# Kernel tuning notes

Measured on AMD Instinct MI355X. Metric: run time of the kernel, lower is better.

## Reference

```python
import jax, jax.numpy as jnp
import numpy as np

B, T, V, C, H, HS, L, DFF = 8192, 8, 65, 512, 8, 64, 6, 2048
LN_EPS = 1e-5


def _layernorm(x, g, b):
    mu = jnp.mean(x, axis=-1, keepdims=True)
    var = jnp.mean(jnp.square(x - mu), axis=-1, keepdims=True)
    return (x - mu) * jax.lax.rsqrt(var + LN_EPS) * g + b


def setup_inputs() -> dict:
    key = jax.random.key(0)
    ks = jax.random.split(key, 16)
    s = 0.02
    inp = {
        "idx": jax.random.randint(ks[0], (B, T), 0, V),
        "tok_table": jax.random.normal(ks[1], (V, C), jnp.float32) * s,
        "pos_table": jax.random.normal(ks[2], (T, C), jnp.float32) * s,
        "wq": jax.random.normal(ks[3], (L, H, C, HS), jnp.float32) * s,
        "wk": jax.random.normal(ks[4], (L, H, C, HS), jnp.float32) * s,
        "wv": jax.random.normal(ks[5], (L, H, C, HS), jnp.float32) * s,
        "proj_w": jax.random.normal(ks[6], (L, C, C), jnp.float32) * s,
        "proj_b": jnp.zeros((L, C), jnp.float32),
        "w1": jax.random.normal(ks[7], (L, C, DFF), jnp.float32) * s,
        "b1": jnp.zeros((L, DFF), jnp.float32),
        "w2": jax.random.normal(ks[8], (L, DFF, C), jnp.float32) * s,
        "b2": jnp.zeros((L, C), jnp.float32),
        "ln1_g": jnp.ones((L, C), jnp.float32),
        "ln1_b": jnp.zeros((L, C), jnp.float32),
        "ln2_g": jnp.ones((L, C), jnp.float32),
        "ln2_b": jnp.zeros((L, C), jnp.float32),
        "lm_w": jax.random.normal(ks[9], (C, V), jnp.float32) * s,
        "lm_b": jnp.zeros((V,), jnp.float32),
    }
    return inp


def reference(idx, tok_table, pos_table, wq, wk, wv, proj_w, proj_b,
              w1, b1, w2, b2, ln1_g, ln1_b, ln2_g, ln2_b, lm_w, lm_b):
    idx = idx[:, -T:]
    x = tok_table[idx] + pos_table[None, :T, :]  # [B,T,C]
    mask = jnp.tril(jnp.ones((T, T), bool))
    scale = C ** (-0.5)  # NOTE: original scales by n_embed, not head_size
    for l in range(L):
        q = jnp.einsum('btc,hcd->bhtd', x, wq[l])
        k = jnp.einsum('btc,hcd->bhtd', x, wk[l])
        v = jnp.einsum('btc,hcd->bhtd', x, wv[l])
        att = jnp.einsum('bhtd,bhsd->bhts', q, k) * scale
        att = jnp.where(mask, att, -jnp.inf)
        att = jax.nn.softmax(att, axis=-1)
        o = jnp.einsum('bhts,bhsd->bhtd', att, v)
        o = o.transpose(0, 2, 1, 3).reshape(x.shape[0], T, C)  # concat heads
        o = o @ proj_w[l] + proj_b[l]
        x = _layernorm(x + o, ln1_g[l], ln1_b[l])  # post-norm
        h = jax.nn.relu(x @ w1[l] + b1[l]) @ w2[l] + b2[l]
        x = _layernorm(x + h, ln2_g[l], ln2_b[l])
    logits = x @ lm_w + lm_b  # [B,T,V]
    return logits
```

## Files before the change

kernel.cpp:

```cpp
#include <hip/hip_runtime.h>
#include <hip/hip_bf16.h>
#include <math.h>

#define NTOK  65536
#define CDIM  512
#define NHEAD 8
#define HSZ   64
#define NLAYER 6
#define DFF   2048
#define VOCAB 65

typedef unsigned short u16;
typedef __attribute__((ext_vector_type(8))) __bf16 bf16x8;
typedef __attribute__((ext_vector_type(4))) float f32x4;
typedef __attribute__((ext_vector_type(8))) unsigned short ushort8;

__device__ __forceinline__ float b2f(u16 u) {
    union { unsigned int i; float f; } x; x.i = ((unsigned int)u) << 16; return x.f;
}
__device__ __forceinline__ u16 f2b(float f) {
    union { float f; unsigned int i; } x; x.f = f;
    unsigned int r = x.i + 0x7fffu + ((x.i >> 16) & 1u);
    return (u16)(r >> 16);
}

__device__ __forceinline__ void async16(const u16* g, u16* l) {
    __builtin_amdgcn_global_load_lds(
        (const __attribute__((address_space(1))) void*)g,
        (__attribute__((address_space(3))) void*)l, 16, 0, 0);
}

template<int EPI>
__global__ __launch_bounds__(512)
void gemm_bt(const u16* __restrict__ A, const u16* __restrict__ Bt,
             void* __restrict__ Cout, const float* __restrict__ bias,
             const u16* __restrict__ res, int K, int lda, int N, int Nout)
{
    __shared__ u16 lA[2 * 256 * 32];
    __shared__ u16 lB[2 * 128 * 32];
    const int tid  = threadIdx.x;

    const int Nx = gridDim.x;
    const int id = blockIdx.y * Nx + blockIdx.x;
    const int xcd = id & 7;
    const int j0  = id >> 3;
    const int mt  = xcd + 8 * (j0 / Nx);
    const int nt  = j0 - (j0 / Nx) * Nx;
    const int m0  = mt * 256;
    const int n0  = nt * 128;

    const int lane = tid & 63;
    const int wv   = tid >> 6;
    const int wr   = (wv >> 1) * 64;
    const int wc   = (wv & 1) * 64;
    const int r16  = lane & 15;
    const int quad = lane >> 4;

    f32x4 acc[4][4] = {};

    const int srow = tid >> 2, skseg = (tid & 3) * 8;
    const u16* pA  = A  + (size_t)(m0 + srow) * lda + skseg;
    const u16* pA2 = pA + (size_t)128 * lda;
    const u16* pB  = Bt + (size_t)(n0 + srow) * K + skseg;
    u16* lAt = &lA[(size_t)tid * 8];
    u16* lBt = &lB[(size_t)tid * 8];

    for (int k0 = 0; k0 < K; k0 += 64) {
        async16(pA  + k0,      lAt);
        async16(pA2 + k0,      lAt + 4096);
        async16(pA  + k0 + 32, lAt + 8192);
        async16(pA2 + k0 + 32, lAt + 12288);
        async16(pB  + k0,      lBt);
        async16(pB  + k0 + 32, lBt + 4096);
        __syncthreads();

#pragma unroll
        for (int s = 0; s < 2; s++) {
            const u16* bA = &lA[s * 8192];
            const u16* bB = &lB[s * 4096];
            bf16x8 af[4], bfr[4];
#pragma unroll
            for (int i = 0; i < 4; i++)
                af[i] = *(const bf16x8*)(const void*)&bA[(wr + i * 16 + r16) * 32 + quad * 8];
#pragma unroll
            for (int j = 0; j < 4; j++)
                bfr[j] = *(const bf16x8*)(const void*)&bB[(wc + j * 16 + r16) * 32 + quad * 8];
#pragma unroll
            for (int j = 0; j < 4; j++)
#pragma unroll
                for (int i = 0; i < 4; i++)
                    acc[j][i] = __builtin_amdgcn_mfma_f32_16x16x32_bf16(bfr[j], af[i], acc[j][i], 0, 0, 0);
        }
        __syncthreads();
    }

#pragma unroll
    for (int i = 0; i < 4; i++) {
        const int row = m0 + wr + i * 16 + r16;
#pragma unroll
        for (int j = 0; j < 4; j++) {
            const int colb = n0 + wc + j * 16 + quad * 4;
            float v[4];
#pragma unroll
            for (int r = 0; r < 4; r++) v[r] = acc[j][i][r];
            if (EPI == 1 || EPI == 2) {
                const f32x4 b4 = *(const f32x4*)(const void*)&bias[colb];
#pragma unroll
                for (int r = 0; r < 4; r++) v[r] += b4[r];
            }
            if (EPI == 1) {
                const uint2 rv = *(const uint2*)(const void*)&res[(size_t)row * N + colb];
                v[0] += b2f((u16)(rv.x & 0xffffu));
                v[1] += b2f((u16)(rv.x >> 16));
                v[2] += b2f((u16)(rv.y & 0xffffu));
                v[3] += b2f((u16)(rv.y >> 16));
            }
            if (EPI == 2) {
#pragma unroll
                for (int r = 0; r < 4; r++) v[r] = fmaxf(v[r], 0.f);
            }
            if (EPI == 3) {
#pragma unroll
                for (int r = 0; r < 4; r++) {
                    const int col = colb + r;
                    if (col < Nout)
                        ((float*)Cout)[(size_t)row * Nout + col] = v[r] + bias[col];
                }
            } else {
                uint2 o;
                o.x = (unsigned)f2b(v[0]) | ((unsigned)f2b(v[1]) << 16);
                o.y = (unsigned)f2b(v[2]) | ((unsigned)f2b(v[3]) << 16);
                *(uint2*)(void*)&((u16*)Cout)[(size_t)row * N + colb] = o;
            }
        }
    }
}

__global__ __launch_bounds__(256)
void attn_k(u16* __restrict__ qkv)
{
    __shared__ float sq[4][8][65], sk[4][8][65], sv[4][8][65], sp[4][64];
    const int w = threadIdx.x >> 6, lane = threadIdx.x & 63;
    const int unit = blockIdx.x * 4 + w;
    const int b = unit >> 3, h = unit & 7;
    const size_t base = (size_t)b * 8 * 1536 + h * 64;
    {
        const int t = lane >> 3, d0 = (lane & 7) * 8;
        const ushort8 q8 = *(const ushort8*)(const void*)&qkv[base + t * 1536 + d0];
        const ushort8 k8 = *(const ushort8*)(const void*)&qkv[base + t * 1536 + 512 + d0];
        const ushort8 v8 = *(const ushort8*)(const void*)&qkv[base + t * 1536 + 1024 + d0];
#pragma unroll
        for (int i = 0; i < 8; i++) {
            sq[w][t][d0 + i] = b2f(q8[i]);
            sk[w][t][d0 + i] = b2f(k8[i]);
            sv[w][t][d0 + i] = b2f(v8[i]);
        }
    }
    __syncthreads();
    const int t = lane >> 3, s = lane & 7;
    float sc = -1e30f;
    if (s <= t) {
        float d = 0.f;
#pragma unroll
        for (int c = 0; c < 64; c++) d += sq[w][t][c] * sk[w][s][c];
        sc = d * 0.04419417382415922f;
    }
    float mx = sc;
#pragma unroll
    for (int m = 1; m < 8; m <<= 1) mx = fmaxf(mx, __shfl_xor(mx, m, 8));
    float e = __expf(sc - mx);
    if (s > t) e = 0.f;
    float sum = e;
#pragma unroll
    for (int m = 1; m < 8; m <<= 1) sum += __shfl_xor(sum, m, 8);
    sp[w][lane] = e / sum;
    __syncthreads();
    {
        const int tt = lane >> 3, d0 = (lane & 7) * 8;
        float a[8] = {};
#pragma unroll
        for (int ss = 0; ss < 8; ss++) {
            const float p = sp[w][tt * 8 + ss];
#pragma unroll
            for (int i = 0; i < 8; i++) a[i] += p * sv[w][ss][d0 + i];
        }
        ushort8 o;
#pragma unroll
        for (int i = 0; i < 8; i++) o[i] = f2b(a[i]);
        *(ushort8*)(void*)&qkv[base + tt * 1536 + d0] = o;
    }
}

__global__ __launch_bounds__(256)
void ln_k(const u16* __restrict__ y, const float* __restrict__ g,
          const float* __restrict__ be, u16* __restrict__ x)
{
    const int w = threadIdx.x >> 6, lane = threadIdx.x & 63;
    const size_t tok = (size_t)blockIdx.x * 4 + w;
    const u16* row = y + tok * 512 + lane * 8;
    ushort8 raw = *(const ushort8*)(const void*)row;
    float v[8];
#pragma unroll
    for (int i = 0; i < 8; i++) v[i] = b2f(raw[i]);
    float s = 0.f;
#pragma unroll
    for (int i = 0; i < 8; i++) s += v[i];
#pragma unroll
    for (int m = 1; m < 64; m <<= 1) s += __shfl_xor(s, m, 64);
    const float mu = s * (1.f / 512.f);
    float q = 0.f;
#pragma unroll
    for (int i = 0; i < 8; i++) { float d = v[i] - mu; q += d * d; }
#pragma unroll
    for (int m = 1; m < 64; m <<= 1) q += __shfl_xor(q, m, 64);
    const float inv = rsqrtf(q * (1.f / 512.f) + 1e-5f);
    f32x4 g0  = *(const f32x4*)(const void*)&g[lane * 8];
    f32x4 g1  = *(const f32x4*)(const void*)&g[lane * 8 + 4];
    f32x4 b0  = *(const f32x4*)(const void*)&be[lane * 8];
    f32x4 b1v = *(const f32x4*)(const void*)&be[lane * 8 + 4];
    ushort8 o;
#pragma unroll
    for (int i = 0; i < 4; i++) o[i]     = f2b((v[i] - mu) * inv * g0[i] + b0[i]);
#pragma unroll
    for (int i = 0; i < 4; i++) o[i + 4] = f2b((v[i + 4] - mu) * inv * g1[i] + b1v[i]);
    *(ushort8*)(void*)&x[tok * 512 + lane * 8] = o;
}

__global__ __launch_bounds__(256)
void embed_k(const int* __restrict__ idx, const float* __restrict__ tokt,
             const float* __restrict__ pos, u16* __restrict__ xb)
{
    const int gid = blockIdx.x * 256 + threadIdx.x;
    const int tk = gid >> 6, seg = (gid & 63) * 8;
    const int t = tk & 7;
    const int ix = idx[tk];
    const f32x4 a0 = *(const f32x4*)(const void*)&tokt[(size_t)ix * 512 + seg];
    const f32x4 a1 = *(const f32x4*)(const void*)&tokt[(size_t)ix * 512 + seg + 4];
    const f32x4 p0 = *(const f32x4*)(const void*)&pos[t * 512 + seg];
    const f32x4 p1 = *(const f32x4*)(const void*)&pos[t * 512 + seg + 4];
    ushort8 o;
#pragma unroll
    for (int i = 0; i < 4; i++) o[i]     = f2b(a0[i] + p0[i]);
#pragma unroll
    for (int i = 0; i < 4; i++) o[i + 4] = f2b(a1[i] + p1[i]);
    *(ushort8*)(void*)&xb[(size_t)tk * 512 + seg] = o;
}

__global__ __launch_bounds__(256)
void conv_t2_k(const float* __restrict__ in, u16* __restrict__ out, int K, int N)
{
    __shared__ float t[32][33];
    const int tx = threadIdx.x & 31, ty4 = (threadIdx.x >> 5) * 4;
    const int n0 = blockIdx.x * 32, k0 = blockIdx.y * 32, l = blockIdx.z;
    const size_t per = (size_t)K * N;
    const float* src = in + l * per;
#pragma unroll
    for (int r = 0; r < 4; r++)
        t[ty4 + r][tx] = src[(size_t)(k0 + ty4 + r) * N + n0 + tx];
    __syncthreads();
    u16* dst = out + l * per;
#pragma unroll
    for (int r = 0; r < 4; r++)
        dst[(size_t)(n0 + ty4 + r) * K + k0 + tx] = f2b(t[tx][ty4 + r]);
}

__global__ __launch_bounds__(256)
void conv_qkv2_k(const float* __restrict__ wq, const float* __restrict__ wk,
                 const float* __restrict__ wv, u16* __restrict__ out)
{
    __shared__ float t[32][33];
    const int tx = threadIdx.x & 31, ty4 = (threadIdx.x >> 5) * 4;
    const int c0 = blockIdx.x * 32, d0 = blockIdx.y * 32;
    const int z = blockIdx.z;
    const int sel = z / 48, rem = z - sel * 48;
    const int l = rem >> 3, h = rem & 7;
    const float* src = (sel == 0) ? wq : (sel == 1) ? wk : wv;
    const float* sb = src + (((size_t)l * 8 + h) * 512) * 64;
#pragma unroll
    for (int r = 0; r < 4; r++)
        t[ty4 + r][tx] = sb[(size_t)(c0 + ty4 + r) * 64 + d0 + tx];
    __syncthreads();
    u16* dst = out + (size_t)l * 786432 + (size_t)(sel * 512 + h * 64 + d0) * 512;
#pragma unroll
    for (int r = 0; r < 4; r++)
        dst[(size_t)(ty4 + r) * 512 + c0 + tx] = f2b(t[tx][ty4 + r]);
}

__global__ __launch_bounds__(256)
void conv_lm_k(const float* __restrict__ lm_w, u16* __restrict__ out)
{
    int gid = blockIdx.x * 256 + threadIdx.x;
    int n = gid >> 9, c = gid & 511;
    out[gid] = (n < VOCAB) ? f2b(lm_w[(size_t)c * VOCAB + n]) : (u16)0;
}

extern "C" void kernel_launch(void* const* d_in, const int* in_sizes, int n_in,
                              void* d_out, int out_size, void* d_ws, size_t ws_size,
                              hipStream_t stream)
{
    const int*   idx    = (const int*)  d_in[0];
    const float* tokt   = (const float*)d_in[1];
    const float* post   = (const float*)d_in[2];
    const float* wq     = (const float*)d_in[3];
    const float* wk     = (const float*)d_in[4];
    const float* wvp    = (const float*)d_in[5];
    const float* proj_w = (const float*)d_in[6];
    const float* proj_b = (const float*)d_in[7];
    const float* w1     = (const float*)d_in[8];
    const float* b1     = (const float*)d_in[9];
    const float* w2     = (const float*)d_in[10];
    const float* b2     = (const float*)d_in[11];
    const float* ln1_g  = (const float*)d_in[12];
    const float* ln1_b  = (const float*)d_in[13];
    const float* ln2_g  = (const float*)d_in[14];
    const float* ln2_b  = (const float*)d_in[15];
    const float* lm_w   = (const float*)d_in[16];
    const float* lm_b   = (const float*)d_in[17];
    float* out = (float*)d_out;

    char* ws = (char*)d_ws;
    u16* wqkvt = (u16*)(ws + 0);
    u16* wprjt = (u16*)(ws + 9437184);
    u16* ww1t  = (u16*)(ws + 12582912);
    u16* ww2t  = (u16*)(ws + 25165824);
    u16* wlmt  = (u16*)(ws + 37748736);
    u16* xb    = (u16*)(ws + 37879808);
    char* big  = ws + 104988672;

    const size_t fixed_bytes = 104988672ull;
    const size_t avail = (ws_size > fixed_bytes) ? (ws_size - fixed_bytes) : 0;
    int chunk_a = 8192, chunk_m = 8192;
    const int cands[3] = {65536, 32768, 16384};
    for (int i = 0; i < 3; i++)
        if ((size_t)cands[i] * 3072ull <= avail) { chunk_a = cands[i]; break; }
    for (int i = 0; i < 3; i++)
        if ((size_t)cands[i] * 4096ull <= avail) { chunk_m = cands[i]; break; }
    const int nca = NTOK / chunk_a, ncm = NTOK / chunk_m;
    u16* qkvc = (u16*)big;
    u16* h1c  = (u16*)big;

    conv_qkv2_k<<<dim3(16, 2, 144), 256, 0, stream>>>(wq, wk, wvp, wqkvt);
    conv_t2_k  <<<dim3(16, 16, 6), 256, 0, stream>>>(proj_w, wprjt, 512, 512);
    conv_t2_k  <<<dim3(64, 16, 6), 256, 0, stream>>>(w1, ww1t, 512, 2048);
    conv_t2_k  <<<dim3(16, 64, 6), 256, 0, stream>>>(w2, ww2t, 2048, 512);
    conv_lm_k  <<<128 * 512 / 256, 256, 0, stream>>>(lm_w, wlmt);

    embed_k<<<NTOK * 64 / 256, 256, 0, stream>>>(idx, tokt, post, xb);

    for (int l = 0; l < NLAYER; l++) {
        for (int c = 0; c < nca; c++) {
            const size_t t0 = (size_t)c * chunk_a;
            gemm_bt<0><<<dim3(12, chunk_a / 256), 512, 0, stream>>>(
                xb + t0 * 512, wqkvt + (size_t)l * 786432, qkvc,
                nullptr, nullptr, 512, 512, 1536, 1536);
            attn_k<<<chunk_a / 4, 256, 0, stream>>>(qkvc);
            gemm_bt<1><<<dim3(4, chunk_a / 256), 512, 0, stream>>>(
                qkvc, wprjt + (size_t)l * 262144, xb + t0 * 512,
                proj_b + l * 512, xb + t0 * 512, 512, 1536, 512, 512);
        }
        ln_k<<<NTOK / 4, 256, 0, stream>>>(xb, ln1_g + l * 512, ln1_b + l * 512, xb);
        for (int c = 0; c < ncm; c++) {
            const size_t t0 = (size_t)c * chunk_m;
            gemm_bt<2><<<dim3(16, chunk_m / 256), 512, 0, stream>>>(
                xb + t0 * 512, ww1t + (size_t)l * 1048576, h1c,
                b1 + l * 2048, nullptr, 512, 512, 2048, 2048);
            gemm_bt<1><<<dim3(4, chunk_m / 256), 512, 0, stream>>>(
                h1c, ww2t + (size_t)l * 1048576, xb + t0 * 512,
                b2 + l * 512, xb + t0 * 512, 2048, 2048, 512, 512);
        }
        ln_k<<<NTOK / 4, 256, 0, stream>>>(xb, ln2_g + l * 512, ln2_b + l * 512, xb);
    }

    gemm_bt<3><<<dim3(1, 256), 512, 0, stream>>>(
        xb, wlmt, out, lm_b, nullptr, 512, 512, 128, VOCAB);
}
```

Before: 3.910 ms.

## Add 256x256-tile GEMM with swizzled LDS, double-buffered prefetch and interleaved MFMA

```diff
diff --git a/kernel.cpp b/kernel.cpp
--- a/kernel.cpp
+++ b/kernel.cpp
@@ -30,76 +30,146 @@
         (__attribute__((address_space(3))) void*)l, 16, 0, 0);
 }
 
+template<int JB, int IB>
+__device__ __forceinline__ void mfma_quad(f32x4 (&acc)[4][8],
+                                          const bf16x8 (&af)[4][2],
+                                          const bf16x8 (&bf)[4][2])
+{
+#pragma unroll
+    for (int kk = 0; kk < 2; kk++)
+#pragma unroll
+        for (int j = 0; j < 2; j++)
+#pragma unroll
+            for (int i = 0; i < 4; i++)
+                acc[JB + j][IB + i] = __builtin_amdgcn_mfma_f32_16x16x32_bf16(
+                    bf[JB + j][kk], af[i][kk], acc[JB + j][IB + i], 0, 0, 0);
+}
+
 template<int EPI>
-__global__ __launch_bounds__(512)
-void gemm_bt(const u16* __restrict__ A, const u16* __restrict__ Bt,
-             void* __restrict__ Cout, const float* __restrict__ bias,
-             const u16* __restrict__ res, int K, int lda, int N, int Nout)
-{
-    __shared__ u16 lA[2 * 256 * 32];
-    __shared__ u16 lB[2 * 128 * 32];
-    const int tid  = threadIdx.x;
+__global__ __launch_bounds__(512, 2)
+void gemm256(const u16* __restrict__ A, const u16* __restrict__ Bt,
+             void* Cout, const float* __restrict__ bias,
+             const u16* res, int K, int lda, int N, int Nout)
+{
+    extern __shared__ __attribute__((aligned(16))) u16 lds[];
+    const int tid = threadIdx.x;
 
     const int Nx = gridDim.x;
     const int id = blockIdx.y * Nx + blockIdx.x;
     const int xcd = id & 7;
-    const int j0  = id >> 3;
-    const int mt  = xcd + 8 * (j0 / Nx);
-    const int nt  = j0 - (j0 / Nx) * Nx;
-    const int m0  = mt * 256;
-    const int n0  = nt * 128;
-
-    const int lane = tid & 63;
-    const int wv   = tid >> 6;
-    const int wr   = (wv >> 1) * 64;
-    const int wc   = (wv & 1) * 64;
-    const int r16  = lane & 15;
-    const int quad = lane >> 4;
-
-    f32x4 acc[4][4] = {};
-
-    const int srow = tid >> 2, skseg = (tid & 3) * 8;
-    const u16* pA  = A  + (size_t)(m0 + srow) * lda + skseg;
-    const u16* pA2 = pA + (size_t)128 * lda;
-    const u16* pB  = Bt + (size_t)(n0 + srow) * K + skseg;
-    u16* lAt = &lA[(size_t)tid * 8];
-    u16* lBt = &lB[(size_t)tid * 8];
-
-    for (int k0 = 0; k0 < K; k0 += 64) {
-        async16(pA  + k0,      lAt);
-        async16(pA2 + k0,      lAt + 4096);
-        async16(pA  + k0 + 32, lAt + 8192);
-        async16(pA2 + k0 + 32, lAt + 12288);
-        async16(pB  + k0,      lBt);
-        async16(pB  + k0 + 32, lBt + 4096);
-        __syncthreads();
-
-#pragma unroll
-        for (int s = 0; s < 2; s++) {
-            const u16* bA = &lA[s * 8192];
-            const u16* bB = &lB[s * 4096];
-            bf16x8 af[4], bfr[4];
-#pragma unroll
-            for (int i = 0; i < 4; i++)
-                af[i] = *(const bf16x8*)(const void*)&bA[(wr + i * 16 + r16) * 32 + quad * 8];
-#pragma unroll
-            for (int j = 0; j < 4; j++)
-                bfr[j] = *(const bf16x8*)(const void*)&bB[(wc + j * 16 + r16) * 32 + quad * 8];
-#pragma unroll
-            for (int j = 0; j < 4; j++)
-#pragma unroll
-                for (int i = 0; i < 4; i++)
-                    acc[j][i] = __builtin_amdgcn_mfma_f32_16x16x32_bf16(bfr[j], af[i], acc[j][i], 0, 0, 0);
-        }
-        __syncthreads();
-    }
-
-#pragma unroll
-    for (int i = 0; i < 4; i++) {
-        const int row = m0 + wr + i * 16 + r16;
+    const int j0 = id >> 3;
+    const int mt = xcd + 8 * (j0 / Nx);
+    const int nt = j0 - (j0 / Nx) * Nx;
+    const int m0 = mt * 256, n0 = nt * 256;
+
+    const int lane = tid & 63, wvv = tid >> 6;
+    const int wvm = wvv >> 2, wvn = wvv & 3;
+    const int r16 = lane & 15, quad = lane >> 4;
+    const int gk0 = quad ^ (r16 & 7);
+    const int g0x8 = gk0 * 8, g1x8 = (gk0 ^ 4) * 8;
+    const int arow = wvm * 128 + r16;
+    const int brow = wvn * 64 + r16;
+
+    const int srow = tid >> 3;
+    const int sg = (tid & 7) ^ (srow & 7);
+    const u16* pA = A + (size_t)(m0 + srow) * lda + sg * 8;
+    const u16* pB = Bt + (size_t)(n0 + srow) * K + sg * 8;
+    u16* const ldst = lds + tid * 8;
+    const size_t ldaq = (size_t)64 * lda, ldah = (size_t)128 * lda;
+    const size_t kq = (size_t)64 * K, kh = (size_t)128 * K;
+
+    const int nk = K >> 6;
+
+    f32x4 acc[4][8] = {};
+    bf16x8 af[4][2], bf[4][2];
+
+#define STAGE_A(c, kt, h) do { \
+    async16(pA + ((h) ? ldah : 0) + (size_t)((kt) * 64),        ldst + (c) * 32768 + (h) * 8192); \
+    async16(pA + ((h) ? ldah : 0) + ldaq + (size_t)((kt) * 64), ldst + (c) * 32768 + (h) * 8192 + 4096); } while (0)
+#define STAGE_B(c, kt, h) do { \
+    async16(pB + ((h) ? kh : 0) + (size_t)((kt) * 64),          ldst + (c) * 32768 + 16384 + (h) * 8192); \
+    async16(pB + ((h) ? kh : 0) + kq + (size_t)((kt) * 64),     ldst + (c) * 32768 + 16384 + (h) * 8192 + 4096); } while (0)
+#define LD_A4(IB0) do { _Pragma("unroll") \
+    for (int i = 0; i < 4; i++) { \
+        const int ro = cb + (arow + ((IB0) + i) * 16) * 64; \
+        af[i][0] = *(const bf16x8*)(const void*)&lds[ro + g0x8]; \
+        af[i][1] = *(const bf16x8*)(const void*)&lds[ro + g1x8]; \
+    } } while (0)
+#define LD_B2(JB0) do { _Pragma("unroll") \
+    for (int j = 0; j < 2; j++) { \
+        const int ro = cb + 16384 + (brow + ((JB0) + j) * 16) * 64; \
+        bf[(JB0) + j][0] = *(const bf16x8*)(const void*)&lds[ro + g0x8]; \
+        bf[(JB0) + j][1] = *(const bf16x8*)(const void*)&lds[ro + g1x8]; \
+    } } while (0)
+#define LGKM0() do { asm volatile("s_waitcnt lgkmcnt(0)" ::: "memory"); \
+                     __builtin_amdgcn_sched_barrier(0); } while (0)
+
+    STAGE_A(0, 0, 0); STAGE_A(0, 0, 1);
+    STAGE_B(0, 0, 0); STAGE_B(0, 0, 1);
+    if (nk > 1) {
+        STAGE_B(1, 1, 0); STAGE_B(1, 1, 1);
+        asm volatile("s_waitcnt vmcnt(4)" ::: "memory");
+    } else {
+        asm volatile("s_waitcnt vmcnt(0)" ::: "memory");
+    }
+    __builtin_amdgcn_s_barrier();
+
+    for (int t = 0; t < nk; ++t) {
+        const int c = t & 1;
+        const int cb = c * 32768;
+
+        LD_A4(0);
+        LD_B2(0);
+        if (t + 1 < nk) STAGE_A(c ^ 1, t + 1, 0);
+        __builtin_amdgcn_s_barrier();
+        LGKM0();
+        __builtin_amdgcn_s_setprio(1);
+        mfma_quad<0, 0>(acc, af, bf);
+        __builtin_amdgcn_s_setprio(0);
+        __builtin_amdgcn_s_barrier();
+
+        LD_B2(2);
+        if (t + 1 < nk) STAGE_A(c ^ 1, t + 1, 1);
+        __builtin_amdgcn_s_barrier();
+        LGKM0();
+        __builtin_amdgcn_s_setprio(1);
+        mfma_quad<2, 0>(acc, af, bf);
+        __builtin_amdgcn_s_setprio(0);
+        __builtin_amdgcn_s_barrier();
+
+        LD_A4(4);
+        if (t + 2 < nk) STAGE_B(c, t + 2, 0);
+        __builtin_amdgcn_s_barrier();
+        LGKM0();
+        __builtin_amdgcn_s_setprio(1);
+        mfma_quad<0, 4>(acc, af, bf);
+        __builtin_amdgcn_s_setprio(0);
+        __builtin_amdgcn_s_barrier();
+
+        if (t + 2 < nk) {
+            STAGE_B(c, t + 2, 1);
+            asm volatile("s_waitcnt vmcnt(4)" ::: "memory");
+        } else {
+            asm volatile("s_waitcnt vmcnt(0)" ::: "memory");
+        }
+        __builtin_amdgcn_s_barrier();
+        __builtin_amdgcn_s_setprio(1);
+        mfma_quad<2, 4>(acc, af, bf);
+        __builtin_amdgcn_s_setprio(0);
+        __builtin_amdgcn_s_barrier();
+    }
+#undef STAGE_A
+#undef STAGE_B
+#undef LD_A4
+#undef LD_B2
+#undef LGKM0
+
+#pragma unroll
+    for (int i = 0; i < 8; i++) {
+        const int row = m0 + wvm * 128 + i * 16 + r16;
 #pragma unroll
         for (int j = 0; j < 4; j++) {
-            const int colb = n0 + wc + j * 16 + quad * 4;
+            const int colb = n0 + wvn * 64 + j * 16 + quad * 4;
             float v[4];
 #pragma unroll
             for (int r = 0; r < 4; r++) v[r] = acc[j][i][r];
@@ -119,6 +189,87 @@
 #pragma unroll
                 for (int r = 0; r < 4; r++) v[r] = fmaxf(v[r], 0.f);
             }
+            uint2 o;
+            o.x = (unsigned)f2b(v[0]) | ((unsigned)f2b(v[1]) << 16);
+            o.y = (unsigned)f2b(v[2]) | ((unsigned)f2b(v[3]) << 16);
+            *(uint2*)(void*)&((u16*)Cout)[(size_t)row * N + colb] = o;
+        }
+    }
+}
+
+template<int EPI>
+__global__ __launch_bounds__(512)
+void gemm_bt(const u16* __restrict__ A, const u16* __restrict__ Bt,
+             void* __restrict__ Cout, const float* __restrict__ bias,
+             const u16* __restrict__ res, int K, int lda, int N, int Nout)
+{
+    __shared__ u16 lA[2 * 256 * 32];
+    __shared__ u16 lB[2 * 128 * 32];
+    const int tid  = threadIdx.x;
+
+    const int Nx = gridDim.x;
+    const int id = blockIdx.y * Nx + blockIdx.x;
+    const int xcd = id & 7;
+    const int j0  = id >> 3;
+    const int mt  = xcd + 8 * (j0 / Nx);
+    const int nt  = j0 - (j0 / Nx) * Nx;
+    const int m0  = mt * 256;
+    const int n0  = nt * 128;
+
+    const int lane = tid & 63;
+    const int wv   = tid >> 6;
+    const int wr   = (wv >> 1) * 64;
+    const int wc   = (wv & 1) * 64;
+    const int r16  = lane & 15;
+    const int quad = lane >> 4;
+
+    f32x4 acc[4][4] = {};
+
+    const int srow = tid >> 2, skseg = (tid & 3) * 8;
+    const u16* pA  = A  + (size_t)(m0 + srow) * lda + skseg;
+    const u16* pA2 = pA + (size_t)128 * lda;
+    const u16* pB  = Bt + (size_t)(n0 + srow) * K + skseg;
+    u16* lAt = &lA[(size_t)tid * 8];
+    u16* lBt = &lB[(size_t)tid * 8];
+
+    for (int k0 = 0; k0 < K; k0 += 64) {
+        async16(pA  + k0,      lAt);
+        async16(pA2 + k0,      lAt + 4096);
+        async16(pA  + k0 + 32, lAt + 8192);
+        async16(pA2 + k0 + 32, lAt + 12288);
+        async16(pB  + k0,      lBt);
+        async16(pB  + k0 + 32, lBt + 4096);
+        __syncthreads();
+
+#pragma unroll
+        for (int s = 0; s < 2; s++) {
+            const u16* bA = &lA[s * 8192];
+            const u16* bB = &lB[s * 4096];
+            bf16x8 af[4], bfr[4];
+#pragma unroll
+            for (int i = 0; i < 4; i++)
+                af[i] = *(const bf16x8*)(const void*)&bA[(wr + i * 16 + r16) * 32 + quad * 8];
+#pragma unroll
+            for (int j = 0; j < 4; j++)
+                bfr[j] = *(const bf16x8*)(const void*)&bB[(wc + j * 16 + r16) * 32 + quad * 8];
+#pragma unroll
+            for (int j = 0; j < 4; j++)
+#pragma unroll
+                for (int i = 0; i < 4; i++)
+                    acc[j][i] = __builtin_amdgcn_mfma_f32_16x16x32_bf16(bfr[j], af[i], acc[j][i], 0, 0, 0);
+        }
+        __syncthreads();
+    }
+
+#pragma unroll
+    for (int i = 0; i < 4; i++) {
+        const int row = m0 + wr + i * 16 + r16;
+#pragma unroll
+        for (int j = 0; j < 4; j++) {
+            const int colb = n0 + wc + j * 16 + quad * 4;
+            float v[4];
+#pragma unroll
+            for (int r = 0; r < 4; r++) v[r] = acc[j][i][r];
             if (EPI == 3) {
 #pragma unroll
                 for (int r = 0; r < 4; r++) {
@@ -318,6 +469,17 @@
     const float* lm_b   = (const float*)d_in[17];
     float* out = (float*)d_out;
 
+    static int smem_set = 0;
+    if (!smem_set) {
+        smem_set = 1;
+        hipFuncSetAttribute(reinterpret_cast<const void*>(&gemm256<0>),
+                            hipFuncAttributeMaxDynamicSharedMemorySize, 131072);
+        hipFuncSetAttribute(reinterpret_cast<const void*>(&gemm256<1>),
+                            hipFuncAttributeMaxDynamicSharedMemorySize, 131072);
+        hipFuncSetAttribute(reinterpret_cast<const void*>(&gemm256<2>),
+                            hipFuncAttributeMaxDynamicSharedMemorySize, 131072);
+    }
+
     char* ws = (char*)d_ws;
     u16* wqkvt = (u16*)(ws + 0);
     u16* wprjt = (u16*)(ws + 9437184);
@@ -350,21 +512,21 @@
     for (int l = 0; l < NLAYER; l++) {
         for (int c = 0; c < nca; c++) {
             const size_t t0 = (size_t)c * chunk_a;
-            gemm_bt<0><<<dim3(12, chunk_a / 256), 512, 0, stream>>>(
+            gemm256<0><<<dim3(6, chunk_a / 256), 512, 131072, stream>>>(
                 xb + t0 * 512, wqkvt + (size_t)l * 786432, qkvc,
                 nullptr, nullptr, 512, 512, 1536, 1536);
             attn_k<<<chunk_a / 4, 256, 0, stream>>>(qkvc);
-            gemm_bt<1><<<dim3(4, chunk_a / 256), 512, 0, stream>>>(
+            gemm256<1><<<dim3(2, chunk_a / 256), 512, 131072, stream>>>(
                 qkvc, wprjt + (size_t)l * 262144, xb + t0 * 512,
                 proj_b + l * 512, xb + t0 * 512, 512, 1536, 512, 512);
         }
         ln_k<<<NTOK / 4, 256, 0, stream>>>(xb, ln1_g + l * 512, ln1_b + l * 512, xb);
         for (int c = 0; c < ncm; c++) {
             const size_t t0 = (size_t)c * chunk_m;
-            gemm_bt<2><<<dim3(16, chunk_m / 256), 512, 0, stream>>>(
+            gemm256<2><<<dim3(8, chunk_m / 256), 512, 131072, stream>>>(
                 xb + t0 * 512, ww1t + (size_t)l * 1048576, h1c,
                 b1 + l * 2048, nullptr, 512, 512, 2048, 2048);
-            gemm_bt<1><<<dim3(4, chunk_m / 256), 512, 0, stream>>>(
+            gemm256<1><<<dim3(2, chunk_m / 256), 512, 131072, stream>>>(
                 h1c, ww2t + (size_t)l * 1048576, xb + t0 * 512,
                 b2 + l * 512, xb + t0 * 512, 2048, 2048, 512, 512);
         }
```

After: 4.115 ms. 1.05x slower.

## Switch transformer GEMMs to 32x32x16 MFMA with XOR-swizzled LDS layout

Applied to the files above, without the earlier changes.

```diff
diff --git a/kernel.cpp b/kernel.cpp
--- a/kernel.cpp
+++ b/kernel.cpp
@@ -13,6 +13,7 @@
 typedef unsigned short u16;
 typedef __attribute__((ext_vector_type(8))) __bf16 bf16x8;
 typedef __attribute__((ext_vector_type(4))) float f32x4;
+typedef __attribute__((ext_vector_type(16))) float f32x16;
 typedef __attribute__((ext_vector_type(8))) unsigned short ushort8;
 
 __device__ __forceinline__ float b2f(u16 u) {
@@ -32,12 +33,12 @@
 
 template<int EPI>
 __global__ __launch_bounds__(512)
-void gemm_bt(const u16* __restrict__ A, const u16* __restrict__ Bt,
-             void* __restrict__ Cout, const float* __restrict__ bias,
-             const u16* __restrict__ res, int K, int lda, int N, int Nout)
-{
-    __shared__ u16 lA[2 * 256 * 32];
-    __shared__ u16 lB[2 * 128 * 32];
+void gemm32(const u16* __restrict__ A, const u16* __restrict__ Bt,
+            void* __restrict__ Cout, const float* __restrict__ bias,
+            const u16* __restrict__ res, int K, int lda, int N)
+{
+    __shared__ u16 lA[256 * 64];
+    __shared__ u16 lB[128 * 64];
     const int tid  = threadIdx.x;
 
     const int Nx = gridDim.x;
@@ -53,6 +54,113 @@
     const int wv   = tid >> 6;
     const int wr   = (wv >> 1) * 64;
     const int wc   = (wv & 1) * 64;
+    const int l31  = lane & 31;
+    const int hi5  = lane >> 5;
+    const int sw   = lane & 7;
+
+    f32x16 acc[2][2] = {};
+
+    const int srow = tid >> 3;
+    const int sg   = ((tid & 7) ^ (srow & 7)) * 8;
+    const u16* pA  = A  + (size_t)(m0 + srow) * lda + sg;
+    const u16* pB  = Bt + (size_t)(n0 + srow) * K + sg;
+    u16* lAt = &lA[(size_t)tid * 8];
+    u16* lBt = &lB[(size_t)tid * 8];
+    const size_t a64 = (size_t)64 * lda, b64 = (size_t)64 * K;
+
+    for (int k0 = 0; k0 < K; k0 += 64) {
+        async16(pA + k0,           lAt);
+        async16(pA + a64 + k0,     lAt + 4096);
+        async16(pA + 2 * a64 + k0, lAt + 8192);
+        async16(pA + 3 * a64 + k0, lAt + 12288);
+        async16(pB + k0,           lBt);
+        async16(pB + b64 + k0,     lBt + 4096);
+        __syncthreads();
+
+        bf16x8 af[2][4], bfr[2][4];
+#pragma unroll
+        for (int rb = 0; rb < 2; rb++)
+#pragma unroll
+            for (int kc = 0; kc < 4; kc++)
+                af[rb][kc] = *(const bf16x8*)(const void*)
+                    &lA[(wr + rb * 32 + l31) * 64 + (((kc * 2 + hi5) ^ sw) * 8)];
+#pragma unroll
+        for (int cb = 0; cb < 2; cb++)
+#pragma unroll
+            for (int kc = 0; kc < 4; kc++)
+                bfr[cb][kc] = *(const bf16x8*)(const void*)
+                    &lB[(wc + cb * 32 + l31) * 64 + (((kc * 2 + hi5) ^ sw) * 8)];
+
+#pragma unroll
+        for (int kc = 0; kc < 4; kc++)
+#pragma unroll
+            for (int cb = 0; cb < 2; cb++)
+#pragma unroll
+                for (int rb = 0; rb < 2; rb++)
+                    acc[cb][rb] = __builtin_amdgcn_mfma_f32_32x32x16_bf16(
+                        bfr[cb][kc], af[rb][kc], acc[cb][rb], 0, 0, 0);
+        __syncthreads();
+    }
+
+#pragma unroll
+    for (int rb = 0; rb < 2; rb++) {
+        const int row = m0 + wr + rb * 32 + l31;
+#pragma unroll
+        for (int cb = 0; cb < 2; cb++) {
+#pragma unroll
+            for (int cg = 0; cg < 4; cg++) {
+                const int colb = n0 + wc + cb * 32 + cg * 8 + hi5 * 4;
+                float v[4];
+#pragma unroll
+                for (int r = 0; r < 4; r++) v[r] = acc[cb][rb][cg * 4 + r];
+                if (EPI == 1 || EPI == 2) {
+                    const f32x4 b4 = *(const f32x4*)(const void*)&bias[colb];
+#pragma unroll
+                    for (int r = 0; r < 4; r++) v[r] += b4[r];
+                }
+                if (EPI == 1) {
+                    const uint2 rv = *(const uint2*)(const void*)&res[(size_t)row * N + colb];
+                    v[0] += b2f((u16)(rv.x & 0xffffu));
+                    v[1] += b2f((u16)(rv.x >> 16));
+                    v[2] += b2f((u16)(rv.y & 0xffffu));
+                    v[3] += b2f((u16)(rv.y >> 16));
+                }
+                if (EPI == 2) {
+#pragma unroll
+                    for (int r = 0; r < 4; r++) v[r] = fmaxf(v[r], 0.f);
+                }
+                uint2 o;
+                o.x = (unsigned)f2b(v[0]) | ((unsigned)f2b(v[1]) << 16);
+                o.y = (unsigned)f2b(v[2]) | ((unsigned)f2b(v[3]) << 16);
+                *(uint2*)(void*)&((u16*)Cout)[(size_t)row * N + colb] = o;
+            }
+        }
+    }
+}
+
+template<int EPI>
+__global__ __launch_bounds__(512)
+void gemm_bt(const u16* __restrict__ A, const u16* __restrict__ Bt,
+             void* __restrict__ Cout, const float* __restrict__ bias,
+             const u16* __restrict__ res, int K, int lda, int N, int Nout)
+{
+    __shared__ u16 lA[2 * 256 * 32];
+    __shared__ u16 lB[2 * 128 * 32];
+    const int tid  = threadIdx.x;
+
+    const int Nx = gridDim.x;
+    const int id = blockIdx.y * Nx + blockIdx.x;
+    const int xcd = id & 7;
+    const int j0  = id >> 3;
+    const int mt  = xcd + 8 * (j0 / Nx);
+    const int nt  = j0 - (j0 / Nx) * Nx;
+    const int m0  = mt * 256;
+    const int n0  = nt * 128;
+
+    const int lane = tid & 63;
+    const int wv   = tid >> 6;
+    const int wr   = (wv >> 1) * 64;
+    const int wc   = (wv & 1) * 64;
     const int r16  = lane & 15;
     const int quad = lane >> 4;
 
@@ -103,22 +211,6 @@
             float v[4];
 #pragma unroll
             for (int r = 0; r < 4; r++) v[r] = acc[j][i][r];
-            if (EPI == 1 || EPI == 2) {
-                const f32x4 b4 = *(const f32x4*)(const void*)&bias[colb];
-#pragma unroll
-                for (int r = 0; r < 4; r++) v[r] += b4[r];
-            }
-            if (EPI == 1) {
-                const uint2 rv = *(const uint2*)(const void*)&res[(size_t)row * N + colb];
-                v[0] += b2f((u16)(rv.x & 0xffffu));
-                v[1] += b2f((u16)(rv.x >> 16));
-                v[2] += b2f((u16)(rv.y & 0xffffu));
-                v[3] += b2f((u16)(rv.y >> 16));
-            }
-            if (EPI == 2) {
-#pragma unroll
-                for (int r = 0; r < 4; r++) v[r] = fmaxf(v[r], 0.f);
-            }
             if (EPI == 3) {
 #pragma unroll
                 for (int r = 0; r < 4; r++) {
@@ -350,23 +442,23 @@
     for (int l = 0; l < NLAYER; l++) {
         for (int c = 0; c < nca; c++) {
             const size_t t0 = (size_t)c * chunk_a;
-            gemm_bt<0><<<dim3(12, chunk_a / 256), 512, 0, stream>>>(
+            gemm32<0><<<dim3(12, chunk_a / 256), 512, 0, stream>>>(
                 xb + t0 * 512, wqkvt + (size_t)l * 786432, qkvc,
-                nullptr, nullptr, 512, 512, 1536, 1536);
+                nullptr, nullptr, 512, 512, 1536);
             attn_k<<<chunk_a / 4, 256, 0, stream>>>(qkvc);
-            gemm_bt<1><<<dim3(4, chunk_a / 256), 512, 0, stream>>>(
+            gemm32<1><<<dim3(4, chunk_a / 256), 512, 0, stream>>>(
                 qkvc, wprjt + (size_t)l * 262144, xb + t0 * 512,
-                proj_b + l * 512, xb + t0 * 512, 512, 1536, 512, 512);
+                proj_b + l * 512, xb + t0 * 512, 512, 1536, 512);
         }
         ln_k<<<NTOK / 4, 256, 0, stream>>>(xb, ln1_g + l * 512, ln1_b + l * 512, xb);
         for (int c = 0; c < ncm; c++) {
             const size_t t0 = (size_t)c * chunk_m;
-            gemm_bt<2><<<dim3(16, chunk_m / 256), 512, 0, stream>>>(
+            gemm32<2><<<dim3(16, chunk_m / 256), 512, 0, stream>>>(
                 xb + t0 * 512, ww1t + (size_t)l * 1048576, h1c,
-                b1 + l * 2048, nullptr, 512, 512, 2048, 2048);
-            gemm_bt<1><<<dim3(4, chunk_m / 256), 512, 0, stream>>>(
+                b1 + l * 2048, nullptr, 512, 512, 2048);
+            gemm32<1><<<dim3(4, chunk_m / 256), 512, 0, stream>>>(
                 h1c, ww2t + (size_t)l * 1048576, xb + t0 * 512,
-                b2 + l * 512, xb + t0 * 512, 2048, 2048, 512, 512);
+                b2 + l * 512, xb + t0 * 512, 2048, 2048, 512);
         }
         ln_k<<<NTOK / 4, 256, 0, stream>>>(xb, ln2_g + l * 512, ln2_b + l * 512, xb);
     }
```

New measurement: 4.586 ms. 17.3% more time.
